# Kernel tuning notes

Measured on AMD Instinct MI355X. Metric: run time of the kernel, lower is better.

Reference implementation:

```python
import jax, jax.numpy as jnp
import numpy as np

DIM = 128
HEADS = 8
RBF_K = 16
N_LIG = 20000
N_PROT = 80000
E = 262144
HEAD_DIM = DIM // HEADS
SCALE = HEAD_DIM ** -0.5


def setup_inputs() -> dict:
    key = jax.random.key(0)
    ks = jax.random.split(key, 16)
    inp = {
        "ligand_x": jax.random.normal(ks[0], (N_LIG, DIM), dtype=jnp.float32),
        "protein_x": jax.random.normal(ks[1], (N_PROT, DIM), dtype=jnp.float32),
        "cross_edges": jax.random.randint(ks[2], (E, 2), 0, N_LIG, dtype=jnp.int64)
        if jax.config.jax_enable_x64 else jax.random.randint(ks[2], (E, 2), 0, N_LIG, dtype=jnp.int32),
        "cross_attr": jax.random.uniform(ks[3], (E, RBF_K), dtype=jnp.float32),
        "Wq": jax.random.normal(ks[4], (DIM, DIM), dtype=jnp.float32) * (DIM ** -0.5),
        "bq": jax.random.normal(ks[5], (DIM,), dtype=jnp.float32) * 0.02,
        "Wk": jax.random.normal(ks[6], (DIM, DIM), dtype=jnp.float32) * (DIM ** -0.5),
        "bk": jax.random.normal(ks[7], (DIM,), dtype=jnp.float32) * 0.02,
        "Wv": jax.random.normal(ks[8], (DIM, DIM), dtype=jnp.float32) * (DIM ** -0.5),
        "bv": jax.random.normal(ks[9], (DIM,), dtype=jnp.float32) * 0.02,
        "Wo": jax.random.normal(ks[10], (DIM, DIM), dtype=jnp.float32) * (DIM ** -0.5),
        "bo": jax.random.normal(ks[11], (DIM,), dtype=jnp.float32) * 0.02,
        "Wr": jax.random.normal(ks[12], (RBF_K, HEADS), dtype=jnp.float32) * (RBF_K ** -0.5),
        "br": jax.random.normal(ks[13], (HEADS,), dtype=jnp.float32) * 0.02,
        "lig_start": 0,
        "prot_start": 0,
    }
    return inp


def _heads(t):
    return t.reshape(t.shape[0], HEADS, HEAD_DIM)


def _cross_attend(q_nodes, k_nodes, v_nodes, dst_idx, src_idx, rbf_bias, n_dst):
    # gather per-edge q/k/v: [E, H, D]
    qe = q_nodes[dst_idx]
    ke = k_nodes[src_idx]
    ve = v_nodes[src_idx]
    logits = jnp.einsum("ehd,ehd->eh", qe, ke) * SCALE + rbf_bias  # [E, H]
    # segment softmax over edges grouped by destination node
    m = jax.ops.segment_max(logits, dst_idx, num_segments=n_dst)  # [N, H]
    ex = jnp.exp(logits - m[dst_idx])
    s = jax.ops.segment_sum(ex, dst_idx, num_segments=n_dst)  # [N, H]
    w = ex / (s[dst_idx] + 1e-8)  # [E, H]
    agg = jax.ops.segment_sum(w[:, :, None] * ve, dst_idx, num_segments=n_dst)
    return agg.reshape(n_dst, HEADS * HEAD_DIM)


def reference(ligand_x, protein_x, cross_edges, cross_attr, Wq, bq, Wk, bk, Wv, bv,
              Wo, bo, Wr, br, lig_start, prot_start):
    n_lig, n_prot = ligand_x.shape[0], protein_x.shape[0]
    q_l = _heads(ligand_x @ Wq + bq)
    k_p = _heads(protein_x @ Wk + bk)
    v_p = _heads(protein_x @ Wv + bv)
    q_p = _heads(protein_x @ Wq + bq)
    k_l = _heads(ligand_x @ Wk + bk)
    v_l = _heads(ligand_x @ Wv + bv)

    lig_local = cross_edges[:, 0] - lig_start
    prot_local = cross_edges[:, 1] - prot_start
    rbf_bias = cross_attr @ Wr + br  # [E, heads]

    lig_agg = _cross_attend(q_l, k_p, v_p, lig_local, prot_local, rbf_bias, n_lig)
    prot_agg = _cross_attend(q_p, k_l, v_l, prot_local, lig_local, rbf_bias, n_prot)

    ligand_out = lig_agg @ Wo + bo   # dropout is identity at inference
    protein_out = prot_agg @ Wo + bo
    return (ligand_out, protein_out)
```

## Files before the change

kernel.cpp:

```cpp
#include <hip/hip_runtime.h>
#include <hip/hip_bf16.h>

typedef unsigned short u16;
typedef __attribute__((ext_vector_type(8))) short short8;
typedef __attribute__((ext_vector_type(4))) float f32x4;

__device__ __forceinline__ float bf2f(u16 u){
  union { unsigned int i; float f; } c; c.i = ((unsigned int)u) << 16; return c.f;
}
__device__ __forceinline__ u16 f2bf(float f){
  union { float f; unsigned int i; } c; c.f = f;
  unsigned int x = c.i;
  return (u16)((x + 0x7FFFu + ((x >> 16) & 1u)) >> 16);
}

__device__ __forceinline__ int edge_get(const int* __restrict__ e32, int i64, int e, int c){
  int idx = 2 * e + c;
  return i64 ? e32[2 * idx] : e32[idx];
}

__global__ void detect_kernel(const u16* __restrict__ lig16,
                              const int* __restrict__ e32, int* __restrict__ flags)
{
  int lane = threadIdx.x;
  int cnt = 0, nz = 0;
  #pragma unroll
  for (int j = 0; j < 4; j++){
    u16 u = lig16[(lane * 4 + j) * 2];
    int ex = (u >> 7) & 0xFF;
    if (ex >= 96 && ex < 160) cnt++;
    if (e32[(lane * 4 + j) * 2 + 1] != 0) nz++;
  }
  #pragma unroll
  for (int off = 1; off < 64; off <<= 1){
    cnt += __shfl_xor(cnt, off);
    nz  += __shfl_xor(nz, off);
  }
  if (lane == 0){
    flags[0] = (cnt < 128) ? 1 : 0;
    flags[1] = (nz == 0) ? 1 : 0;
  }
}

__global__ __launch_bounds__(256) void prep_w(
    const void* __restrict__ Wq, const void* __restrict__ Wk,
    const void* __restrict__ Wv, const void* __restrict__ Wo,
    const void* __restrict__ bq, const void* __restrict__ bk,
    const void* __restrict__ bv, const void* __restrict__ bo,
    u16* __restrict__ Wt, float* __restrict__ biasP, const int* __restrict__ flags)
{
  int mat = blockIdx.x, tid = threadIdx.x;
  const void* W = (mat == 0) ? Wq : (mat == 1) ? Wk : (mat == 2) ? Wv : Wo;
  const void* b = (mat == 0) ? bq : (mat == 1) ? bk : (mat == 2) ? bv : bo;
  int F = flags[0];
  u16* dst = Wt + mat * 16384;
  #pragma unroll 4
  for (int j = 0; j < 64; j++){
    int idx = tid + j * 256;
    u16 w = F ? f2bf(((const float*)W)[idx]) : ((const u16*)W)[idx];
    dst[(idx & 127) * 128 + (idx >> 7)] = w;
  }
  if (tid < 128)
    biasP[mat * 128 + tid] = F ? ((const float*)b)[tid] : bf2f(((const u16*)b)[tid]);
}

__global__ __launch_bounds__(256) void gemm_multi(
    const void* __restrict__ A0, int M0, const void* __restrict__ A1, int M1, int mb0,
    const u16* __restrict__ Wt, const float* __restrict__ biasP, int wbase, int nm,
    u16* __restrict__ O0b, u16* __restrict__ O1b, u16* __restrict__ O2b,
    float* __restrict__ O0f,
    int a_force_bf16, int final_out, const int* __restrict__ flags)
{
  __shared__ __align__(16) u16 As[64][136];
  __shared__ __align__(16) u16 Fs[64][136];

  int tid = threadIdx.x;
  int F = flags[0];
  int AF = a_force_bf16 ? 0 : F;
  int TT = mb0 + ((M1 + 63) >> 6);
  int bx = blockIdx.x;
  int mat = bx / TT;
  int tt  = bx - mat * TT;

  const void* A; int M, m0, orow;
  if (tt < mb0){ A = A0; M = M0; m0 = tt * 64;          orow = m0; }
  else         { A = A1; M = M1; m0 = (tt - mb0) * 64;  orow = M0 + m0; }

  if (AF){
    const float* Af = (const float*)A;
    #pragma unroll
    for (int j = 0; j < 8; j++){
      int u = tid + j * 256, row = u >> 5, c4 = (u & 31) * 4;
      float4 v = make_float4(0.f, 0.f, 0.f, 0.f);
      if (m0 + row < M) v = *(const float4*)&Af[(size_t)(m0 + row) * 128 + c4];
      ushort4 o; o.x = f2bf(v.x); o.y = f2bf(v.y); o.z = f2bf(v.z); o.w = f2bf(v.w);
      *(ushort4*)&As[row][c4] = o;
    }
  } else {
    const float4* Au = (const float4*)A;
    #pragma unroll
    for (int j = 0; j < 4; j++){
      int u = tid + j * 256, row = u >> 4, c8 = (u & 15);
      float4 v = make_float4(0.f, 0.f, 0.f, 0.f);
      if (m0 + row < M) v = Au[(size_t)(m0 + row) * 16 + c8];
      *(float4*)&As[row][c8 * 8] = v;
    }
  }
  __syncthreads();

  int wave = tid >> 6, lane = tid & 63;
  int quad = lane >> 4, ml = lane & 15;
  int f32out = final_out && F;

  const u16* wp = Wt + (size_t)(wbase + mat) * 16384
                    + (size_t)(wave * 32 + ml) * 128 + quad * 8;
  short8 wf0[4], wf1[4];
  #pragma unroll
  for (int kk = 0; kk < 4; kk++){
    wf0[kk] = *(const short8*)&wp[kk * 32];
    wf1[kk] = *(const short8*)&wp[2048 + kk * 32];
  }
  float b0 = biasP[(wbase + mat) * 128 + wave * 32 + ml];
  float b1 = biasP[(wbase + mat) * 128 + wave * 32 + 16 + ml];

  f32x4 acc[4][2];
  #pragma unroll
  for (int mt = 0; mt < 4; mt++){
    acc[mt][0] = (f32x4){0.f, 0.f, 0.f, 0.f};
    acc[mt][1] = (f32x4){0.f, 0.f, 0.f, 0.f};
  }

  #pragma unroll
  for (int mt = 0; mt < 4; mt++){
    #pragma unroll
    for (int kk = 0; kk < 4; kk++){
      short8 af = *(const short8*)&As[mt * 16 + ml][kk * 32 + quad * 8];
      acc[mt][0] = __builtin_amdgcn_mfma_f32_16x16x32_bf16(af, wf0[kk], acc[mt][0], 0, 0, 0);
      acc[mt][1] = __builtin_amdgcn_mfma_f32_16x16x32_bf16(af, wf1[kk], acc[mt][1], 0, 0, 0);
    }
  }

  if (f32out){
    #pragma unroll
    for (int mt = 0; mt < 4; mt++){
      #pragma unroll
      for (int r = 0; r < 4; r++){
        int row = mt * 16 + quad * 4 + r;
        if (m0 + row < M){
          float* op = &O0f[(size_t)(orow + row) * 128 + wave * 32 + ml];
          op[0]  = acc[mt][0][r] + b0;
          op[16] = acc[mt][1][r] + b1;
        }
      }
    }
  } else {
    #pragma unroll
    for (int mt = 0; mt < 4; mt++){
      #pragma unroll
      for (int r = 0; r < 4; r++){
        int row = mt * 16 + quad * 4 + r;
        Fs[row][wave * 32 + ml]      = f2bf(acc[mt][0][r] + b0);
        Fs[row][wave * 32 + 16 + ml] = f2bf(acc[mt][1][r] + b1);
      }
    }
    __syncthreads();
    u16* Cb = (mat == 0) ? O0b : ((mat == 1) ? O1b : O2b);
    #pragma unroll
    for (int j = 0; j < 4; j++){
      int u = tid + j * 256, row = u >> 4, c8 = (u & 15) * 8;
      if (m0 + row < M)
        *(short8*)&Cb[(size_t)(orow + row) * 128 + c8] = *(const short8*)&Fs[row][c8];
    }
  }
}

__global__ __launch_bounds__(256) void edge_pre(
    const void* __restrict__ attr, const void* __restrict__ Wr,
    const void* __restrict__ br, float* __restrict__ ebias,
    const int* __restrict__ edges, const int* __restrict__ ls_p,
    const int* __restrict__ ps_p, int* __restrict__ cnt, int nlig, int E_,
    const int* __restrict__ flags)
{
  __shared__ float w[16][8];
  __shared__ float b[8];
  int tid = threadIdx.x;
  int F = flags[0];
  if (tid < 128) w[tid >> 3][tid & 7] = F ? ((const float*)Wr)[tid] : bf2f(((const u16*)Wr)[tid]);
  if (tid < 8)   b[tid] = F ? ((const float*)br)[tid] : bf2f(((const u16*)br)[tid]);
  __syncthreads();
  int e = blockIdx.x * 256 + tid;
  if (e >= E_) return;

  int I64 = flags[1];
  int dl = edge_get(edges, I64, e, 0) - ls_p[0];
  int dp = edge_get(edges, I64, e, 1) - ps_p[0];
  atomicAdd(&cnt[dl], 1);
  atomicAdd(&cnt[nlig + dp], 1);

  float a[16];
  if (F){
    const float* af = (const float*)attr;
    #pragma unroll
    for (int j = 0; j < 4; j++){
      float4 t = *(const float4*)&af[e * 16 + j * 4];
      a[4*j] = t.x; a[4*j+1] = t.y; a[4*j+2] = t.z; a[4*j+3] = t.w;
    }
  } else {
    const u16* au = (const u16*)attr;
    #pragma unroll
    for (int j = 0; j < 4; j++){
      ushort4 t = *(const ushort4*)&au[e * 16 + j * 4];
      a[4*j] = bf2f(t.x); a[4*j+1] = bf2f(t.y); a[4*j+2] = bf2f(t.z); a[4*j+3] = bf2f(t.w);
    }
  }
  #pragma unroll
  for (int hh = 0; hh < 8; hh++){
    float s = b[hh];
    #pragma unroll
    for (int r = 0; r < 16; r++) s += a[r] * w[r][hh];
    ebias[e * 8 + hh] = s;
  }
}

__global__ __launch_bounds__(256) void scan_blocksum(
    const int* __restrict__ cnt, int* __restrict__ bsum, int n)
{
  __shared__ int red[4];
  int tid = threadIdx.x;
  int i = blockIdx.x * 256 + tid;
  int v = (i < n) ? cnt[i] : 0;
  #pragma unroll
  for (int off = 1; off < 64; off <<= 1) v += __shfl_xor(v, off);
  if ((tid & 63) == 0) red[tid >> 6] = v;
  __syncthreads();
  if (tid == 0) bsum[blockIdx.x] = red[0] + red[1] + red[2] + red[3];
}

__global__ __launch_bounds__(512) void scan_bsum(
    int* __restrict__ bsum, int* __restrict__ boff, int nb)
{
  __shared__ int buf[512];
  int tid = threadIdx.x;
  int v = (tid < nb) ? bsum[tid] : 0;
  buf[tid] = v; __syncthreads();
  for (int off = 1; off < 512; off <<= 1){
    int t = (tid >= off) ? buf[tid - off] : 0;
    __syncthreads();
    buf[tid] += t;
    __syncthreads();
  }
  if (tid < nb) boff[tid] = buf[tid] - v;
}

__global__ __launch_bounds__(256) void scan_final(
    const int* __restrict__ cnt, const int* __restrict__ boff,
    int* __restrict__ offs, int* __restrict__ cursor, int n)
{
  __shared__ int buf[256];
  int tid = threadIdx.x;
  int i = blockIdx.x * 256 + tid;
  int v = (i < n) ? cnt[i] : 0;
  buf[tid] = v; __syncthreads();
  for (int off = 1; off < 256; off <<= 1){
    int t = (tid >= off) ? buf[tid - off] : 0;
    __syncthreads();
    buf[tid] += t;
    __syncthreads();
  }
  int excl = buf[tid] - v + boff[blockIdx.x];
  if (i < n){
    offs[i] = excl;
    cursor[i] = excl;
    if (i == n - 1) offs[n] = excl + v;
  }
}

__global__ __launch_bounds__(256) void scatter_kernel(
    const int* __restrict__ edges, const int* __restrict__ ls_p,
    const int* __restrict__ ps_p, int* __restrict__ cursor,
    int2* __restrict__ sorted, int nlig, int E_,
    const int* __restrict__ flags)
{
  int e = blockIdx.x * 256 + threadIdx.x;
  if (e >= E_) return;
  int I64 = flags[1];
  int dl = edge_get(edges, I64, e, 0) - ls_p[0];
  int dp = edge_get(edges, I64, e, 1) - ps_p[0];
  int p1 = atomicAdd(&cursor[dl], 1);        sorted[p1] = make_int2(e, nlig + dp);
  int p2 = atomicAdd(&cursor[nlig + dp], 1); sorted[p2] = make_int2(e, dl);
}

__global__ __launch_bounds__(256) void attn_kernel(
    const u16* __restrict__ Q, const u16* __restrict__ K, const u16* __restrict__ V,
    const int2* __restrict__ sorted, const int* __restrict__ offs,
    const float* __restrict__ ebias, u16* __restrict__ AGG, int ntot)
{
  int t = blockIdx.x * 4 + (threadIdx.x >> 6);
  if (t >= ntot) return;
  int lane = threadIdx.x & 63;
  int ql = lane & 15;
  int q4 = lane >> 4;
  int h  = ql >> 1;

  int beg = offs[t], end = offs[t + 1];

  if (beg == end){
    if (lane < 16){
      short8 z = {0, 0, 0, 0, 0, 0, 0, 0};
      *(short8*)&AGG[(size_t)t * 128 + ql * 8] = z;
    }
    return;
  }

  short8 qv = *(const short8*)&Q[(size_t)t * 128 + ql * 8];
  float qf[8];
  #pragma unroll
  for (int j = 0; j < 8; j++) qf[j] = bf2f((u16)qv[j]);

  float m = -1e30f, l = 0.f;
  float a[8];
  #pragma unroll
  for (int j = 0; j < 8; j++) a[j] = 0.f;

  int i = beg + q4;
  int2 cur = make_int2(0, 0), nxt = make_int2(0, 0);
  if (i < end)     cur = sorted[i];
  if (i + 4 < end) nxt = sorted[i + 4];

  short8 kA = {0,0,0,0,0,0,0,0}, vA = {0,0,0,0,0,0,0,0};
  float ebA = 0.f;
  if (i < end){
    kA = *(const short8*)&K[(size_t)cur.y * 128 + ql * 8];
    vA = *(const short8*)&V[(size_t)cur.y * 128 + ql * 8];
    ebA = ebias[(size_t)cur.x * 8 + h];
  }

  while (i < end){
    short8 kB = {0,0,0,0,0,0,0,0}, vB = {0,0,0,0,0,0,0,0};
    float ebB = 0.f;
    if (i + 4 < end){
      kB = *(const short8*)&K[(size_t)nxt.y * 128 + ql * 8];
      vB = *(const short8*)&V[(size_t)nxt.y * 128 + ql * 8];
      ebB = ebias[(size_t)nxt.x * 8 + h];
    }
    int2 n2 = make_int2(0, 0);
    if (i + 8 < end) n2 = sorted[i + 8];

    float s = 0.f;
    #pragma unroll
    for (int j = 0; j < 8; j++) s += qf[j] * bf2f((u16)kA[j]);
    s += __shfl_xor(s, 1);
    float logit = s * 0.25f + ebA;
    float nm = fmaxf(m, logit);
    float alpha = __expf(m - nm);
    float p = __expf(logit - nm);
    #pragma unroll
    for (int j = 0; j < 8; j++) a[j] = a[j] * alpha + p * bf2f((u16)vA[j]);
    l = l * alpha + p;
    m = nm;

    kA = kB; vA = vB; ebA = ebB;
    cur = nxt; nxt = n2;
    i += 4;
  }

  #pragma unroll
  for (int mask = 16; mask <= 32; mask <<= 1){
    float mo = __shfl_xor(m, mask);
    float lo = __shfl_xor(l, mask);
    float nm = fmaxf(m, mo);
    float sA = __expf(m - nm);
    float sB = __expf(mo - nm);
    l = l * sA + lo * sB;
    #pragma unroll
    for (int j = 0; j < 8; j++){
      float ao = __shfl_xor(a[j], mask);
      a[j] = a[j] * sA + ao * sB;
    }
    m = nm;
  }

  if (lane < 16){
    float inv = 1.f / (l + 1e-8f);
    short8 o;
    #pragma unroll
    for (int j = 0; j < 8; j++) o[j] = (short)f2bf(a[j] * inv);
    *(short8*)&AGG[(size_t)t * 128 + ql * 8] = o;
  }
}

extern "C" void kernel_launch(void* const* d_in, const int* in_sizes, int n_in,
                              void* d_out, int out_size, void* d_ws, size_t ws_size,
                              hipStream_t stream)
{
  const void* ligand_x  = d_in[0];
  const void* protein_x = d_in[1];
  const int* edges      = (const int*)d_in[2];
  const void* attr      = d_in[3];
  const void* Wq = d_in[4];  const void* bq = d_in[5];
  const void* Wk = d_in[6];  const void* bk = d_in[7];
  const void* Wv = d_in[8];  const void* bv = d_in[9];
  const void* Wo = d_in[10]; const void* bo = d_in[11];
  const void* Wr = d_in[12]; const void* br = d_in[13];
  const int* ls_p = (const int*)d_in[14];
  const int* ps_p = (const int*)d_in[15];

  const int nlig = in_sizes[0] / 128;
  const int nprot = in_sizes[1] / 128;
  const int E = in_sizes[2] / 2;
  const int ntot = nlig + nprot;

  char* w = (char*)d_ws;
  size_t off = 0;
  auto alloc = [&](size_t bytes) -> void* {
    void* p = w + off;
    off = (off + bytes + 255) & ~(size_t)255;
    return p;
  };
  int*   flags = (int*)alloc(256);
  u16*   Wt    = (u16*)alloc(4 * 16384 * 2);
  float* biasP = (float*)alloc(4 * 128 * 4);
  u16* Qb  = (u16*)alloc((size_t)ntot * 128 * 2);
  u16* Kb  = (u16*)alloc((size_t)ntot * 128 * 2);
  u16* Vb  = (u16*)alloc((size_t)ntot * 128 * 2);
  u16* AGG = (u16*)alloc((size_t)ntot * 128 * 2);
  float* ebias = (float*)alloc((size_t)E * 8 * 4);
  int* cnt    = (int*)alloc((size_t)ntot * 4);
  int* offs   = (int*)alloc((size_t)(ntot + 1) * 4);
  int* cursor = (int*)alloc((size_t)ntot * 4);
  int* bsum   = (int*)alloc(512 * 4);
  int* boff   = (int*)alloc(512 * 4);
  int2* sorted = (int2*)alloc((size_t)2 * E * 8);
  (void)ws_size; (void)n_in; (void)out_size;

  const int mb_l = (nlig + 63) / 64;
  const int mb_p = (nprot + 63) / 64;
  const int mb_t = (ntot + 63) / 64;
  const int eb = (E + 255) / 256;
  const int nb = (ntot + 255) / 256;

  hipMemsetAsync(cnt, 0, (size_t)ntot * 4, stream);
  detect_kernel<<<1, 64, 0, stream>>>((const u16*)ligand_x, edges, flags);
  prep_w<<<4, 256, 0, stream>>>(Wq, Wk, Wv, Wo, bq, bk, bv, bo, Wt, biasP, flags);

  gemm_multi<<<3 * (mb_l + mb_p), 256, 0, stream>>>(
      ligand_x, nlig, protein_x, nprot, mb_l,
      Wt, biasP, 0, 3,
      Qb, Kb, Vb, nullptr, 0, 0, flags);

  edge_pre<<<eb, 256, 0, stream>>>(attr, Wr, br, ebias, edges, ls_p, ps_p,
                                   cnt, nlig, E, flags);

  scan_blocksum<<<nb, 256, 0, stream>>>(cnt, bsum, ntot);
  scan_bsum<<<1, 512, 0, stream>>>(bsum, boff, nb);
  scan_final<<<nb, 256, 0, stream>>>(cnt, boff, offs, cursor, ntot);
  scatter_kernel<<<eb, 256, 0, stream>>>(edges, ls_p, ps_p, cursor, sorted, nlig, E, flags);

  attn_kernel<<<(ntot + 3) / 4, 256, 0, stream>>>(Qb, Kb, Vb, sorted, offs, ebias, AGG, ntot);

  gemm_multi<<<mb_t, 256, 0, stream>>>(
      AGG, ntot, nullptr, 0, mb_t,
      Wt, biasP, 3, 1,
      (u16*)d_out, nullptr, nullptr, (float*)d_out,
      1, 1, flags);
}
```

Measured before the change: 336.5 us.

## Fuse QKV with edge bias, output projection into attention, memset into init

Merges the memset and dtype-detect kernels into one init kernel. Interleaves the QKV GEMM tiles and the edge-bias blocks in a single launch, with each GEMM tile loading its input rows once and computing all three projections. Folds the Wo projection into the attention kernel through a small shared-memory tile, which removes the AGG buffer round trip and one GEMM launch. In exchange, every attention block reloads its Wo slice from cache, and the fused MFMA uses only 4 of its 16 rows, which wastes matrix throughput.

```diff
diff --git a/kernel.cpp b/kernel.cpp
--- a/kernel.cpp
+++ b/kernel.cpp
@@ -19,26 +19,34 @@
   return i64 ? e32[2 * idx] : e32[idx];
 }
 
-__global__ void detect_kernel(const u16* __restrict__ lig16,
-                              const int* __restrict__ e32, int* __restrict__ flags)
-{
-  int lane = threadIdx.x;
-  int cnt = 0, nz = 0;
-  #pragma unroll
-  for (int j = 0; j < 4; j++){
-    u16 u = lig16[(lane * 4 + j) * 2];
-    int ex = (u >> 7) & 0xFF;
-    if (ex >= 96 && ex < 160) cnt++;
-    if (e32[(lane * 4 + j) * 2 + 1] != 0) nz++;
-  }
-  #pragma unroll
-  for (int off = 1; off < 64; off <<= 1){
-    cnt += __shfl_xor(cnt, off);
-    nz  += __shfl_xor(nz, off);
-  }
-  if (lane == 0){
-    flags[0] = (cnt < 128) ? 1 : 0;
-    flags[1] = (nz == 0) ? 1 : 0;
+__global__ __launch_bounds__(256) void init_kernel(
+    const u16* __restrict__ lig16, const int* __restrict__ e32,
+    int* __restrict__ flags, int* __restrict__ cnt, int ntot)
+{
+  int tid = threadIdx.x;
+  if (blockIdx.x == 0){
+    if (tid < 64){
+      int c = 0, nz = 0;
+      #pragma unroll
+      for (int j = 0; j < 4; j++){
+        u16 u = lig16[(tid * 4 + j) * 2];
+        int ex = (u >> 7) & 0xFF;
+        if (ex >= 96 && ex < 160) c++;
+        if (e32[(tid * 4 + j) * 2 + 1] != 0) nz++;
+      }
+      #pragma unroll
+      for (int off = 1; off < 64; off <<= 1){
+        c  += __shfl_xor(c, off);
+        nz += __shfl_xor(nz, off);
+      }
+      if (tid == 0){
+        flags[0] = (c < 128) ? 1 : 0;
+        flags[1] = (nz == 0) ? 1 : 0;
+      }
+    }
+  } else {
+    int i = (blockIdx.x - 1) * 256 + tid;
+    if (i < ntot) cnt[i] = 0;
   }
 }
 
@@ -64,161 +72,147 @@
     biasP[mat * 128 + tid] = F ? ((const float*)b)[tid] : bf2f(((const u16*)b)[tid]);
 }
 
-__global__ __launch_bounds__(256) void gemm_multi(
+__global__ __launch_bounds__(256) void fat_qkv_ep(
     const void* __restrict__ A0, int M0, const void* __restrict__ A1, int M1, int mb0,
-    const u16* __restrict__ Wt, const float* __restrict__ biasP, int wbase, int nm,
+    const u16* __restrict__ Wt, const float* __restrict__ biasP,
     u16* __restrict__ O0b, u16* __restrict__ O1b, u16* __restrict__ O2b,
-    float* __restrict__ O0f,
-    int a_force_bf16, int final_out, const int* __restrict__ flags)
-{
-  __shared__ __align__(16) u16 As[64][136];
-  __shared__ __align__(16) u16 Fs[64][136];
-
-  int tid = threadIdx.x;
-  int F = flags[0];
-  int AF = a_force_bf16 ? 0 : F;
-  int TT = mb0 + ((M1 + 63) >> 6);
-  int bx = blockIdx.x;
-  int mat = bx / TT;
-  int tt  = bx - mat * TT;
-
-  const void* A; int M, m0, orow;
-  if (tt < mb0){ A = A0; M = M0; m0 = tt * 64;          orow = m0; }
-  else         { A = A1; M = M1; m0 = (tt - mb0) * 64;  orow = M0 + m0; }
-
-  if (AF){
-    const float* Af = (const float*)A;
-    #pragma unroll
-    for (int j = 0; j < 8; j++){
-      int u = tid + j * 256, row = u >> 5, c4 = (u & 31) * 4;
-      float4 v = make_float4(0.f, 0.f, 0.f, 0.f);
-      if (m0 + row < M) v = *(const float4*)&Af[(size_t)(m0 + row) * 128 + c4];
-      ushort4 o; o.x = f2bf(v.x); o.y = f2bf(v.y); o.z = f2bf(v.z); o.w = f2bf(v.w);
-      *(ushort4*)&As[row][c4] = o;
-    }
-  } else {
-    const float4* Au = (const float4*)A;
-    #pragma unroll
-    for (int j = 0; j < 4; j++){
-      int u = tid + j * 256, row = u >> 4, c8 = (u & 15);
-      float4 v = make_float4(0.f, 0.f, 0.f, 0.f);
-      if (m0 + row < M) v = Au[(size_t)(m0 + row) * 16 + c8];
-      *(float4*)&As[row][c8 * 8] = v;
-    }
-  }
-  __syncthreads();
-
-  int wave = tid >> 6, lane = tid & 63;
-  int quad = lane >> 4, ml = lane & 15;
-  int f32out = final_out && F;
-
-  const u16* wp = Wt + (size_t)(wbase + mat) * 16384
-                    + (size_t)(wave * 32 + ml) * 128 + quad * 8;
-  short8 wf0[4], wf1[4];
-  #pragma unroll
-  for (int kk = 0; kk < 4; kk++){
-    wf0[kk] = *(const short8*)&wp[kk * 32];
-    wf1[kk] = *(const short8*)&wp[2048 + kk * 32];
-  }
-  float b0 = biasP[(wbase + mat) * 128 + wave * 32 + ml];
-  float b1 = biasP[(wbase + mat) * 128 + wave * 32 + 16 + ml];
-
-  f32x4 acc[4][2];
-  #pragma unroll
-  for (int mt = 0; mt < 4; mt++){
-    acc[mt][0] = (f32x4){0.f, 0.f, 0.f, 0.f};
-    acc[mt][1] = (f32x4){0.f, 0.f, 0.f, 0.f};
-  }
-
-  #pragma unroll
-  for (int mt = 0; mt < 4; mt++){
-    #pragma unroll
-    for (int kk = 0; kk < 4; kk++){
-      short8 af = *(const short8*)&As[mt * 16 + ml][kk * 32 + quad * 8];
-      acc[mt][0] = __builtin_amdgcn_mfma_f32_16x16x32_bf16(af, wf0[kk], acc[mt][0], 0, 0, 0);
-      acc[mt][1] = __builtin_amdgcn_mfma_f32_16x16x32_bf16(af, wf1[kk], acc[mt][1], 0, 0, 0);
-    }
-  }
-
-  if (f32out){
-    #pragma unroll
-    for (int mt = 0; mt < 4; mt++){
-      #pragma unroll
-      for (int r = 0; r < 4; r++){
-        int row = mt * 16 + quad * 4 + r;
-        if (m0 + row < M){
-          float* op = &O0f[(size_t)(orow + row) * 128 + wave * 32 + ml];
-          op[0]  = acc[mt][0][r] + b0;
-          op[16] = acc[mt][1][r] + b1;
-        }
-      }
-    }
-  } else {
-    #pragma unroll
-    for (int mt = 0; mt < 4; mt++){
-      #pragma unroll
-      for (int r = 0; r < 4; r++){
-        int row = mt * 16 + quad * 4 + r;
-        Fs[row][wave * 32 + ml]      = f2bf(acc[mt][0][r] + b0);
-        Fs[row][wave * 32 + 16 + ml] = f2bf(acc[mt][1][r] + b1);
-      }
-    }
-    __syncthreads();
-    u16* Cb = (mat == 0) ? O0b : ((mat == 1) ? O1b : O2b);
-    #pragma unroll
-    for (int j = 0; j < 4; j++){
-      int u = tid + j * 256, row = u >> 4, c8 = (u & 15) * 8;
-      if (m0 + row < M)
-        *(short8*)&Cb[(size_t)(orow + row) * 128 + c8] = *(const short8*)&Fs[row][c8];
-    }
-  }
-}
-
-__global__ __launch_bounds__(256) void edge_pre(
     const void* __restrict__ attr, const void* __restrict__ Wr,
     const void* __restrict__ br, float* __restrict__ ebias,
     const int* __restrict__ edges, const int* __restrict__ ls_p,
-    const int* __restrict__ ps_p, int* __restrict__ cnt, int nlig, int E_,
-    const int* __restrict__ flags)
-{
-  __shared__ float w[16][8];
-  __shared__ float b[8];
+    const int* __restrict__ ps_p, int* __restrict__ cnt,
+    int nlig, int E_, const int* __restrict__ flags)
+{
+  __shared__ __align__(16) char smem[34816];
   int tid = threadIdx.x;
   int F = flags[0];
-  if (tid < 128) w[tid >> 3][tid & 7] = F ? ((const float*)Wr)[tid] : bf2f(((const u16*)Wr)[tid]);
-  if (tid < 8)   b[tid] = F ? ((const float*)br)[tid] : bf2f(((const u16*)br)[tid]);
-  __syncthreads();
-  int e = blockIdx.x * 256 + tid;
-  if (e >= E_) return;
-
-  int I64 = flags[1];
-  int dl = edge_get(edges, I64, e, 0) - ls_p[0];
-  int dp = edge_get(edges, I64, e, 1) - ps_p[0];
-  atomicAdd(&cnt[dl], 1);
-  atomicAdd(&cnt[nlig + dp], 1);
-
-  float a[16];
-  if (F){
-    const float* af = (const float*)attr;
+
+  int TT = mb0 + ((M1 + 63) >> 6);
+  int eb = (E_ + 255) >> 8;
+  int G  = TT + eb;
+  int bx = blockIdx.x;
+  long long pp = (long long)bx * TT;
+  int tile = (int)(pp / G);
+  int isQ  = (int)(((long long)(bx + 1) * TT) / G) > tile;
+
+  if (isQ){
+    u16 (*As)[136] = (u16(*)[136])smem;
+    u16 (*Fs)[136] = (u16(*)[136])(smem + 17408);
+    int AF = F;
+    const void* A; int M, m0, orow;
+    if (tile < mb0){ A = A0; M = M0; m0 = tile * 64;          orow = m0; }
+    else           { A = A1; M = M1; m0 = (tile - mb0) * 64;  orow = M0 + m0; }
+
+    if (AF){
+      const float* Af = (const float*)A;
+      #pragma unroll
+      for (int j = 0; j < 8; j++){
+        int u = tid + j * 256, row = u >> 5, c4 = (u & 31) * 4;
+        float4 v = make_float4(0.f, 0.f, 0.f, 0.f);
+        if (m0 + row < M) v = *(const float4*)&Af[(size_t)(m0 + row) * 128 + c4];
+        ushort4 o; o.x = f2bf(v.x); o.y = f2bf(v.y); o.z = f2bf(v.z); o.w = f2bf(v.w);
+        *(ushort4*)&As[row][c4] = o;
+      }
+    } else {
+      const float4* Au = (const float4*)A;
+      #pragma unroll
+      for (int j = 0; j < 4; j++){
+        int u = tid + j * 256, row = u >> 4, c8 = (u & 15);
+        float4 v = make_float4(0.f, 0.f, 0.f, 0.f);
+        if (m0 + row < M) v = Au[(size_t)(m0 + row) * 16 + c8];
+        *(float4*)&As[row][c8 * 8] = v;
+      }
+    }
+    __syncthreads();
+
+    int wave = tid >> 6, lane = tid & 63;
+    int quad = lane >> 4, ml = lane & 15;
+
+    for (int mat = 0; mat < 3; mat++){
+      const u16* wp = Wt + (size_t)mat * 16384
+                        + (size_t)(wave * 32 + ml) * 128 + quad * 8;
+      short8 wf0[4], wf1[4];
+      #pragma unroll
+      for (int kk = 0; kk < 4; kk++){
+        wf0[kk] = *(const short8*)&wp[kk * 32];
+        wf1[kk] = *(const short8*)&wp[2048 + kk * 32];
+      }
+      float b0 = biasP[mat * 128 + wave * 32 + ml];
+      float b1 = biasP[mat * 128 + wave * 32 + 16 + ml];
+
+      f32x4 acc[4][2];
+      #pragma unroll
+      for (int mt = 0; mt < 4; mt++){
+        acc[mt][0] = (f32x4){0.f, 0.f, 0.f, 0.f};
+        acc[mt][1] = (f32x4){0.f, 0.f, 0.f, 0.f};
+      }
+      #pragma unroll
+      for (int mt = 0; mt < 4; mt++){
+        #pragma unroll
+        for (int kk = 0; kk < 4; kk++){
+          short8 af = *(const short8*)&As[mt * 16 + ml][kk * 32 + quad * 8];
+          acc[mt][0] = __builtin_amdgcn_mfma_f32_16x16x32_bf16(af, wf0[kk], acc[mt][0], 0, 0, 0);
+          acc[mt][1] = __builtin_amdgcn_mfma_f32_16x16x32_bf16(af, wf1[kk], acc[mt][1], 0, 0, 0);
+        }
+      }
+
+      if (mat > 0) __syncthreads();
+      #pragma unroll
+      for (int mt = 0; mt < 4; mt++){
+        #pragma unroll
+        for (int r = 0; r < 4; r++){
+          int row = mt * 16 + quad * 4 + r;
+          Fs[row][wave * 32 + ml]      = f2bf(acc[mt][0][r] + b0);
+          Fs[row][wave * 32 + 16 + ml] = f2bf(acc[mt][1][r] + b1);
+        }
+      }
+      __syncthreads();
+      u16* Cb = (mat == 0) ? O0b : ((mat == 1) ? O1b : O2b);
+      #pragma unroll
+      for (int j = 0; j < 4; j++){
+        int u = tid + j * 256, row = u >> 4, c8 = (u & 15) * 8;
+        if (m0 + row < M)
+          *(short8*)&Cb[(size_t)(orow + row) * 128 + c8] = *(const short8*)&Fs[row][c8];
+      }
+    }
+  } else {
+    int eidx = bx - tile;
+    float (*w)[8] = (float(*)[8])smem;
+    float* b = (float*)(smem + 512);
+    if (tid < 128) w[tid >> 3][tid & 7] = F ? ((const float*)Wr)[tid] : bf2f(((const u16*)Wr)[tid]);
+    if (tid < 8)   b[tid] = F ? ((const float*)br)[tid] : bf2f(((const u16*)br)[tid]);
+    __syncthreads();
+    int e = eidx * 256 + tid;
+    if (e >= E_) return;
+
+    int I64 = flags[1];
+    int dl = edge_get(edges, I64, e, 0) - ls_p[0];
+    int dp = edge_get(edges, I64, e, 1) - ps_p[0];
+    atomicAdd(&cnt[dl], 1);
+    atomicAdd(&cnt[nlig + dp], 1);
+
+    float a[16];
+    if (F){
+      const float* af = (const float*)attr;
+      #pragma unroll
+      for (int j = 0; j < 4; j++){
+        float4 t = *(const float4*)&af[e * 16 + j * 4];
+        a[4*j] = t.x; a[4*j+1] = t.y; a[4*j+2] = t.z; a[4*j+3] = t.w;
+      }
+    } else {
+      const u16* au = (const u16*)attr;
+      #pragma unroll
+      for (int j = 0; j < 4; j++){
+        ushort4 t = *(const ushort4*)&au[e * 16 + j * 4];
+        a[4*j] = bf2f(t.x); a[4*j+1] = bf2f(t.y); a[4*j+2] = bf2f(t.z); a[4*j+3] = bf2f(t.w);
+      }
+    }
     #pragma unroll
-    for (int j = 0; j < 4; j++){
-      float4 t = *(const float4*)&af[e * 16 + j * 4];
-      a[4*j] = t.x; a[4*j+1] = t.y; a[4*j+2] = t.z; a[4*j+3] = t.w;
-    }
-  } else {
-    const u16* au = (const u16*)attr;
-    #pragma unroll
-    for (int j = 0; j < 4; j++){
-      ushort4 t = *(const ushort4*)&au[e * 16 + j * 4];
-      a[4*j] = bf2f(t.x); a[4*j+1] = bf2f(t.y); a[4*j+2] = bf2f(t.z); a[4*j+3] = bf2f(t.w);
-    }
-  }
-  #pragma unroll
-  for (int hh = 0; hh < 8; hh++){
-    float s = b[hh];
-    #pragma unroll
-    for (int r = 0; r < 16; r++) s += a[r] * w[r][hh];
-    ebias[e * 8 + hh] = s;
+    for (int hh = 0; hh < 8; hh++){
+      float s = b[hh];
+      #pragma unroll
+      for (int r = 0; r < 16; r++) s += a[r] * w[r][hh];
+      ebias[e * 8 + hh] = s;
+    }
   }
 }
 
@@ -290,102 +284,142 @@
   int p2 = atomicAdd(&cursor[nlig + dp], 1); sorted[p2] = make_int2(e, dl);
 }
 
-__global__ __launch_bounds__(256) void attn_kernel(
+__global__ __launch_bounds__(256) void attn_out(
     const u16* __restrict__ Q, const u16* __restrict__ K, const u16* __restrict__ V,
     const int2* __restrict__ sorted, const int* __restrict__ offs,
-    const float* __restrict__ ebias, u16* __restrict__ AGG, int ntot)
-{
-  int t = blockIdx.x * 4 + (threadIdx.x >> 6);
-  if (t >= ntot) return;
+    const float* __restrict__ ebias, const u16* __restrict__ Wt,
+    const float* __restrict__ biasP, void* __restrict__ OUT, int ntot,
+    const int* __restrict__ flags)
+{
+  __shared__ __align__(16) u16 aggS[4][136];
+
+  int wid = threadIdx.x >> 6;
+  int t = blockIdx.x * 4 + wid;
   int lane = threadIdx.x & 63;
   int ql = lane & 15;
   int q4 = lane >> 4;
   int h  = ql >> 1;
 
-  int beg = offs[t], end = offs[t + 1];
-
-  if (beg == end){
-    if (lane < 16){
-      short8 z = {0, 0, 0, 0, 0, 0, 0, 0};
-      *(short8*)&AGG[(size_t)t * 128 + ql * 8] = z;
-    }
-    return;
-  }
-
-  short8 qv = *(const short8*)&Q[(size_t)t * 128 + ql * 8];
-  float qf[8];
-  #pragma unroll
-  for (int j = 0; j < 8; j++) qf[j] = bf2f((u16)qv[j]);
+  int beg = 0, end = 0;
+  if (t < ntot){ beg = offs[t]; end = offs[t + 1]; }
 
   float m = -1e30f, l = 0.f;
   float a[8];
   #pragma unroll
   for (int j = 0; j < 8; j++) a[j] = 0.f;
 
-  int i = beg + q4;
-  int2 cur = make_int2(0, 0), nxt = make_int2(0, 0);
-  if (i < end)     cur = sorted[i];
-  if (i + 4 < end) nxt = sorted[i + 4];
-
-  short8 kA = {0,0,0,0,0,0,0,0}, vA = {0,0,0,0,0,0,0,0};
-  float ebA = 0.f;
-  if (i < end){
-    kA = *(const short8*)&K[(size_t)cur.y * 128 + ql * 8];
-    vA = *(const short8*)&V[(size_t)cur.y * 128 + ql * 8];
-    ebA = ebias[(size_t)cur.x * 8 + h];
-  }
-
-  while (i < end){
-    short8 kB = {0,0,0,0,0,0,0,0}, vB = {0,0,0,0,0,0,0,0};
-    float ebB = 0.f;
-    if (i + 4 < end){
-      kB = *(const short8*)&K[(size_t)nxt.y * 128 + ql * 8];
-      vB = *(const short8*)&V[(size_t)nxt.y * 128 + ql * 8];
-      ebB = ebias[(size_t)nxt.x * 8 + h];
-    }
-    int2 n2 = make_int2(0, 0);
-    if (i + 8 < end) n2 = sorted[i + 8];
-
-    float s = 0.f;
+  if (beg < end){
+    short8 qv = *(const short8*)&Q[(size_t)t * 128 + ql * 8];
+    float qf[8];
     #pragma unroll
-    for (int j = 0; j < 8; j++) s += qf[j] * bf2f((u16)kA[j]);
-    s += __shfl_xor(s, 1);
-    float logit = s * 0.25f + ebA;
-    float nm = fmaxf(m, logit);
-    float alpha = __expf(m - nm);
-    float p = __expf(logit - nm);
+    for (int j = 0; j < 8; j++) qf[j] = bf2f((u16)qv[j]);
+
+    int i = beg + q4;
+    int2 cur = make_int2(0, 0), nxt = make_int2(0, 0);
+    if (i < end)     cur = sorted[i];
+    if (i + 4 < end) nxt = sorted[i + 4];
+
+    short8 kA = {0,0,0,0,0,0,0,0}, vA = {0,0,0,0,0,0,0,0};
+    float ebA = 0.f;
+    if (i < end){
+      kA = *(const short8*)&K[(size_t)cur.y * 128 + ql * 8];
+      vA = *(const short8*)&V[(size_t)cur.y * 128 + ql * 8];
+      ebA = ebias[(size_t)cur.x * 8 + h];
+    }
+
+    while (i < end){
+      short8 kB = {0,0,0,0,0,0,0,0}, vB = {0,0,0,0,0,0,0,0};
+      float ebB = 0.f;
+      if (i + 4 < end){
+        kB = *(const short8*)&K[(size_t)nxt.y * 128 + ql * 8];
+        vB = *(const short8*)&V[(size_t)nxt.y * 128 + ql * 8];
+        ebB = ebias[(size_t)nxt.x * 8 + h];
+      }
+      int2 n2 = make_int2(0, 0);
+      if (i + 8 < end) n2 = sorted[i + 8];
+
+      float s = 0.f;
+      #pragma unroll
+      for (int j = 0; j < 8; j++) s += qf[j] * bf2f((u16)kA[j]);
+      s += __shfl_xor(s, 1);
+      float logit = s * 0.25f + ebA;
+      float nm = fmaxf(m, logit);
+      float alpha = __expf(m - nm);
+      float p = __expf(logit - nm);
+      #pragma unroll
+      for (int j = 0; j < 8; j++) a[j] = a[j] * alpha + p * bf2f((u16)vA[j]);
+      l = l * alpha + p;
+      m = nm;
+
+      kA = kB; vA = vB; ebA = ebB;
+      cur = nxt; nxt = n2;
+      i += 4;
+    }
+
     #pragma unroll
-    for (int j = 0; j < 8; j++) a[j] = a[j] * alpha + p * bf2f((u16)vA[j]);
-    l = l * alpha + p;
-    m = nm;
-
-    kA = kB; vA = vB; ebA = ebB;
-    cur = nxt; nxt = n2;
-    i += 4;
-  }
-
+    for (int mask = 16; mask <= 32; mask <<= 1){
+      float mo = __shfl_xor(m, mask);
+      float lo = __shfl_xor(l, mask);
+      float nm = fmaxf(m, mo);
+      float sA = __expf(m - nm);
+      float sB = __expf(mo - nm);
+      l = l * sA + lo * sB;
+      #pragma unroll
+      for (int j = 0; j < 8; j++){
+        float ao = __shfl_xor(a[j], mask);
+        a[j] = a[j] * sA + ao * sB;
+      }
+      m = nm;
+    }
+  }
+
+  if (lane < 16){
+    short8 o = {0, 0, 0, 0, 0, 0, 0, 0};
+    if (beg < end){
+      float inv = 1.f / (l + 1e-8f);
+      #pragma unroll
+      for (int j = 0; j < 8; j++) o[j] = (short)f2bf(a[j] * inv);
+    }
+    *(short8*)&aggS[wid][ql * 8] = o;
+  }
+  __syncthreads();
+
+  const u16* wp = Wt + (size_t)3 * 16384 + (size_t)(wid * 32 + ql) * 128 + q4 * 8;
+  short8 wf0[4], wf1[4];
   #pragma unroll
-  for (int mask = 16; mask <= 32; mask <<= 1){
-    float mo = __shfl_xor(m, mask);
-    float lo = __shfl_xor(l, mask);
-    float nm = fmaxf(m, mo);
-    float sA = __expf(m - nm);
-    float sB = __expf(mo - nm);
-    l = l * sA + lo * sB;
+  for (int kk = 0; kk < 4; kk++){
+    wf0[kk] = *(const short8*)&wp[kk * 32];
+    wf1[kk] = *(const short8*)&wp[2048 + kk * 32];
+  }
+  float b0 = biasP[3 * 128 + wid * 32 + ql];
+  float b1 = biasP[3 * 128 + wid * 32 + 16 + ql];
+
+  f32x4 acc0 = (f32x4){0.f, 0.f, 0.f, 0.f};
+  f32x4 acc1 = (f32x4){0.f, 0.f, 0.f, 0.f};
+  #pragma unroll
+  for (int kk = 0; kk < 4; kk++){
+    short8 af = *(const short8*)&aggS[ql & 3][kk * 32 + q4 * 8];
+    acc0 = __builtin_amdgcn_mfma_f32_16x16x32_bf16(af, wf0[kk], acc0, 0, 0, 0);
+    acc1 = __builtin_amdgcn_mfma_f32_16x16x32_bf16(af, wf1[kk], acc1, 0, 0, 0);
+  }
+
+  if (q4 == 0){
+    int F = flags[0];
     #pragma unroll
-    for (int j = 0; j < 8; j++){
-      float ao = __shfl_xor(a[j], mask);
-      a[j] = a[j] * sA + ao * sB;
-    }
-    m = nm;
-  }
-
-  if (lane < 16){
-    float inv = 1.f / (l + 1e-8f);
-    short8 o;
-    #pragma unroll
-    for (int j = 0; j < 8; j++) o[j] = (short)f2bf(a[j] * inv);
-    *(short8*)&AGG[(size_t)t * 128 + ql * 8] = o;
+    for (int r = 0; r < 4; r++){
+      int tr = blockIdx.x * 4 + r;
+      if (tr < ntot){
+        if (F){
+          float* op = (float*)OUT + (size_t)tr * 128 + wid * 32 + ql;
+          op[0]  = acc0[r] + b0;
+          op[16] = acc1[r] + b1;
+        } else {
+          u16* op = (u16*)OUT + (size_t)tr * 128 + wid * 32 + ql;
+          op[0]  = f2bf(acc0[r] + b0);
+          op[16] = f2bf(acc1[r] + b1);
+        }
+      }
+    }
   }
 }
 
@@ -423,7 +457,6 @@
   u16* Qb  = (u16*)alloc((size_t)ntot * 128 * 2);
   u16* Kb  = (u16*)alloc((size_t)ntot * 128 * 2);
   u16* Vb  = (u16*)alloc((size_t)ntot * 128 * 2);
-  u16* AGG = (u16*)alloc((size_t)ntot * 128 * 2);
   float* ebias = (float*)alloc((size_t)E * 8 * 4);
   int* cnt    = (int*)alloc((size_t)ntot * 4);
   int* offs   = (int*)alloc((size_t)(ntot + 1) * 4);
@@ -435,32 +468,24 @@
 
   const int mb_l = (nlig + 63) / 64;
   const int mb_p = (nprot + 63) / 64;
-  const int mb_t = (ntot + 63) / 64;
   const int eb = (E + 255) / 256;
   const int nb = (ntot + 255) / 256;
 
-  hipMemsetAsync(cnt, 0, (size_t)ntot * 4, stream);
-  detect_kernel<<<1, 64, 0, stream>>>((const u16*)ligand_x, edges, flags);
+  init_kernel<<<nb + 1, 256, 0, stream>>>((const u16*)ligand_x, edges, flags, cnt, ntot);
+
   prep_w<<<4, 256, 0, stream>>>(Wq, Wk, Wv, Wo, bq, bk, bv, bo, Wt, biasP, flags);
 
-  gemm_multi<<<3 * (mb_l + mb_p), 256, 0, stream>>>(
+  const int TT = mb_l + mb_p;
+  fat_qkv_ep<<<TT + eb, 256, 0, stream>>>(
       ligand_x, nlig, protein_x, nprot, mb_l,
-      Wt, biasP, 0, 3,
-      Qb, Kb, Vb, nullptr, 0, 0, flags);
-
-  edge_pre<<<eb, 256, 0, stream>>>(attr, Wr, br, ebias, edges, ls_p, ps_p,
-                                   cnt, nlig, E, flags);
+      Wt, biasP, Qb, Kb, Vb,
+      attr, Wr, br, ebias, edges, ls_p, ps_p, cnt, nlig, E, flags);
 
   scan_blocksum<<<nb, 256, 0, stream>>>(cnt, bsum, ntot);
   scan_bsum<<<1, 512, 0, stream>>>(bsum, boff, nb);
   scan_final<<<nb, 256, 0, stream>>>(cnt, boff, offs, cursor, ntot);
   scatter_kernel<<<eb, 256, 0, stream>>>(edges, ls_p, ps_p, cursor, sorted, nlig, E, flags);
 
-  attn_kernel<<<(ntot + 3) / 4, 256, 0, stream>>>(Qb, Kb, Vb, sorted, offs, ebias, AGG, ntot);
-
-  gemm_multi<<<mb_t, 256, 0, stream>>>(
-      AGG, ntot, nullptr, 0, mb_t,
-      Wt, biasP, 3, 1,
-      (u16*)d_out, nullptr, nullptr, (float*)d_out,
-      1, 1, flags);
-}
+  attn_out<<<(ntot + 3) / 4, 256, 0, stream>>>(
+      Qb, Kb, Vb, sorted, offs, ebias, Wt, biasP, d_out, ntot, flags);
+}
```

Result: slower. 380.2 us (+13.0%).
